# Optimization experiments

Hardware: AMD Instinct MI355X
Metric: run time of the kernel (lower is better)

## Reference

```python
import jax, jax.numpy as jnp
import numpy as np

GAMMA = 1.0
INPUT_DIM = 512
NUM_CENTERS = 4096
BATCH = 16384


def setup_inputs() -> dict:
    key = jax.random.key(0)
    kx, kc = jax.random.split(key)
    x = jax.random.normal(kx, (BATCH, INPUT_DIM), dtype=jnp.float32)
    centers = jax.random.normal(kc, (NUM_CENTERS, INPUT_DIM), dtype=jnp.float32)
    return {"x": x, "centers": centers}


def reference(x, centers):
    x_sq = jnp.sum(x * x, axis=-1, keepdims=True)            # [B, 1]
    c_sq = jnp.sum(centers * centers, axis=-1)               # [C]
    cross = jnp.einsum("bd,cd->bc", x, centers)              # [B, C]
    dist_sq = x_sq - 2.0 * cross + c_sq[None, :]
    return jnp.exp(-GAMMA * dist_sq)
```

## Files before the change

### kernel.cpp

```cpp
#include <hip/hip_runtime.h>
#include <stdint.h>

#define M_DIM 16384
#define N_DIM 4096
#define K_DIM 512

#define BM 128
#define BN 256
#define BK 128

typedef int v8i __attribute__((ext_vector_type(8)));
typedef float f32x16 __attribute__((ext_vector_type(16)));

typedef __attribute__((address_space(3))) uint32_t lds_u32_t;
typedef const __attribute__((address_space(1))) uint32_t glob_u32_t;

__device__ __forceinline__ void gload16(const void* g, void* l) {
    __builtin_amdgcn_global_load_lds((glob_u32_t*)g, (lds_u32_t*)l, 16, 0, 0);
}

__global__ __launch_bounds__(256)
void convert_norm_kernel(const float* __restrict__ X, const float* __restrict__ C,
                         uint8_t* __restrict__ Xf8, uint8_t* __restrict__ Cf8,
                         float* __restrict__ xsq, float* __restrict__ csq) {
    const int wave = threadIdx.x >> 6;
    const int lane = threadIdx.x & 63;
    const int row = blockIdx.x * 4 + wave;
    const float* src;
    uint8_t* dst;
    float* nrm;
    int r;
    if (row < M_DIM) { src = X; dst = Xf8; nrm = xsq; r = row; }
    else             { src = C; dst = Cf8; nrm = csq; r = row - M_DIM; }

    const float4* p = (const float4*)(src + (size_t)r * K_DIM) + lane * 2;
    float4 a = p[0], b = p[1];
    uint32_t lo = 0, hi = 0;
    lo = __builtin_amdgcn_cvt_pk_fp8_f32(a.x, a.y, lo, false);
    lo = __builtin_amdgcn_cvt_pk_fp8_f32(a.z, a.w, lo, true);
    hi = __builtin_amdgcn_cvt_pk_fp8_f32(b.x, b.y, hi, false);
    hi = __builtin_amdgcn_cvt_pk_fp8_f32(b.z, b.w, hi, true);
    *(uint2*)(dst + (size_t)r * K_DIM + lane * 8) = make_uint2(lo, hi);

    float s = a.x*a.x + a.y*a.y + a.z*a.z + a.w*a.w
            + b.x*b.x + b.y*b.y + b.z*b.z + b.w*b.w;
    #pragma unroll
    for (int off = 32; off > 0; off >>= 1) s += __shfl_down(s, off, 64);
    if (lane == 0) nrm[r] = s;
}

__global__ __launch_bounds__(256, 2)
void rbf_mfma_kernel(const uint8_t* __restrict__ A8, const uint8_t* __restrict__ B8,
                     const float* __restrict__ xsq, const float* __restrict__ csq,
                     float* __restrict__ out) {
    __shared__ uint8_t As[BM * BK];
    __shared__ uint8_t Bs[BN * BK];

    const int tid  = threadIdx.x;
    const int lane = tid & 63;
    const int wave = tid >> 6;
    const int h    = lane >> 5;
    const int r31  = lane & 31;

    const int bn = (blockIdx.x & 15) * BN;
    const int bm = (blockIdx.x >> 4) * BM;

    const int wm = (wave >> 1) * 64;
    const int wn = (wave & 1) * 128;

    const int sr  = tid >> 3;
    const int skc = ((tid & 7) - sr) & 7;
    const uint8_t* pA = A8 + (size_t)(bm + sr) * K_DIM + skc * 16;
    const uint8_t* pB = B8 + (size_t)(bn + sr) * K_DIM + skc * 16;
    uint8_t* AsW = As + wave * 1024;
    uint8_t* BsW = Bs + wave * 1024;

    f32x16 acc[2][4] = {};

    for (int k0 = 0; k0 < K_DIM; k0 += BK) {
        #pragma unroll
        for (int R = 0; R < 4; ++R)
            gload16(pA + k0 + (size_t)R * 32 * K_DIM, AsW + R * 4096);
        #pragma unroll
        for (int R = 0; R < 8; ++R)
            gload16(pB + k0 + (size_t)R * 32 * K_DIM, BsW + R * 4096);
        __syncthreads();

        #pragma unroll
        for (int ks = 0; ks < 2; ++ks) {
            v8i av[2], bv[4];
            #pragma unroll
            for (int i = 0; i < 2; ++i) {
                const int panel = (wm >> 5) + i;
                uint4 lo = *(const uint4*)(As + (panel * 256 + r31 * 8 + ((ks * 4 + 2 * h + 0 + r31) & 7)) * 16);
                uint4 hi = *(const uint4*)(As + (panel * 256 + r31 * 8 + ((ks * 4 + 2 * h + 1 + r31) & 7)) * 16);
                av[i] = (v8i){(int)lo.x, (int)lo.y, (int)lo.z, (int)lo.w,
                              (int)hi.x, (int)hi.y, (int)hi.z, (int)hi.w};
            }
            #pragma unroll
            for (int j = 0; j < 4; ++j) {
                const int panel = (wn >> 5) + j;
                uint4 lo = *(const uint4*)(Bs + (panel * 256 + r31 * 8 + ((ks * 4 + 2 * h + 0 + r31) & 7)) * 16);
                uint4 hi = *(const uint4*)(Bs + (panel * 256 + r31 * 8 + ((ks * 4 + 2 * h + 1 + r31) & 7)) * 16);
                bv[j] = (v8i){(int)lo.x, (int)lo.y, (int)lo.z, (int)lo.w,
                              (int)hi.x, (int)hi.y, (int)hi.z, (int)hi.w};
            }
            #pragma unroll
            for (int i = 0; i < 2; ++i)
                #pragma unroll
                for (int j = 0; j < 4; ++j)
                    acc[i][j] = __builtin_amdgcn_mfma_scale_f32_32x32x64_f8f6f4(
                        av[i], bv[j], acc[i][j],
                        0 , 0 ,
                        0, 0x7F7F7F7Fu ,
                        0, 0x7F7F7F7Fu );
        }
        __syncthreads();
    }

    float cs[4];
    #pragma unroll
    for (int j = 0; j < 4; ++j) cs[j] = csq[bn + wn + 32 * j + r31];

    #pragma unroll
    for (int i = 0; i < 2; ++i) {
        #pragma unroll
        for (int r = 0; r < 16; ++r) {
            const int gm = bm + wm + 32 * i + 4 * h + (r & 3) + 8 * (r >> 2);
            const float xs = xsq[gm];
            float* orow = out + (size_t)gm * N_DIM + bn + wn;
            #pragma unroll
            for (int j = 0; j < 4; ++j) {
                float d = xs - 2.0f * acc[i][j][r] + cs[j];
                orow[32 * j + r31] = __expf(-d);
            }
        }
    }
}

extern "C" void kernel_launch(void* const* d_in, const int* in_sizes, int n_in,
                              void* d_out, int out_size, void* d_ws, size_t ws_size,
                              hipStream_t stream) {
    const float* X = (const float*)d_in[0];
    const float* C = (const float*)d_in[1];
    float* out = (float*)d_out;

    uint8_t* Xf8 = (uint8_t*)d_ws;
    uint8_t* Cf8 = Xf8 + (size_t)M_DIM * K_DIM;
    float* xsq = (float*)(Cf8 + (size_t)N_DIM * K_DIM);
    float* csq = xsq + M_DIM;

    convert_norm_kernel<<<(M_DIM + N_DIM) / 4, 256, 0, stream>>>(X, C, Xf8, Cf8, xsq, csq);
    rbf_mfma_kernel<<<(M_DIM / BM) * (N_DIM / BN), 256, 0, stream>>>(Xf8, Cf8, xsq, csq, out);
}
```

Baseline: 308.9 us.

## Double-buffer LDS K-tiles and permute B rows for float4 output stores

Halves the K tile to 64 and double-buffers the A and B LDS tiles, so the next tile's global-to-LDS loads are issued before the current tile's MFMAs. This is meant to hide load latency and drops one barrier per iteration. B rows are loaded in a permuted order so each lane owns four consecutive output columns, letting the epilogue read csq with one float4 and write the output with 128-bit stores. The risk is more loop iterations with less work each, and LDS swizzle or row-mapping mistakes.

```diff
diff --git a/kernel.cpp b/kernel.cpp
--- a/kernel.cpp
+++ b/kernel.cpp
@@ -7,7 +7,7 @@
 
 #define BM 128
 #define BN 256
-#define BK 128
+#define BK 64
 
 typedef int v8i __attribute__((ext_vector_type(8)));
 typedef float f32x16 __attribute__((ext_vector_type(16)));
@@ -53,8 +53,8 @@
 void rbf_mfma_kernel(const uint8_t* __restrict__ A8, const uint8_t* __restrict__ B8,
                      const float* __restrict__ xsq, const float* __restrict__ csq,
                      float* __restrict__ out) {
-    __shared__ uint8_t As[BM * BK];
-    __shared__ uint8_t Bs[BN * BK];
+    __shared__ uint8_t As[2 * BM * BK];
+    __shared__ uint8_t Bs[2 * BN * BK];
 
     const int tid  = threadIdx.x;
     const int lane = tid & 63;
@@ -68,59 +68,78 @@
     const int wm = (wave >> 1) * 64;
     const int wn = (wave & 1) * 128;
 
-    const int sr  = tid >> 3;
-    const int skc = ((tid & 7) - sr) & 7;
-    const uint8_t* pA = A8 + (size_t)(bm + sr) * K_DIM + skc * 16;
-    const uint8_t* pB = B8 + (size_t)(bn + sr) * K_DIM + skc * 16;
-    uint8_t* AsW = As + wave * 1024;
-    uint8_t* BsW = Bs + wave * 1024;
+    const int tr = tid >> 2;
+    const int tc = tid & 3;
+    const int cc = (tc - tr) & 3;
+    const int b7 = tid >> 7;
+
+    const uint8_t* gA0 = A8 + (size_t)(bm + tr) * K_DIM + cc * 16;
+    const uint8_t* gA1 = gA0 + (size_t)64 * K_DIM;
+    const int brow = 4 * (tr & 31);
+    const uint8_t* gB[4];
+    #pragma unroll
+    for (int R = 0; R < 4; ++R) {
+        const int p = 2 * R + b7;
+        const int grow = bn + (p >> 2) * 128 + brow + (p & 3);
+        gB[R] = B8 + (size_t)grow * K_DIM + cc * 16;
+    }
+
+    {
+        uint8_t* aD = As + wave * 1024;
+        uint8_t* bD = Bs + wave * 1024;
+        gload16(gA0, aD);
+        gload16(gA1, aD + 4096);
+        #pragma unroll
+        for (int R = 0; R < 4; ++R) gload16(gB[R], bD + R * 4096);
+    }
+    int koff = 64;
+
+    const int s0 = ((2 * h + 0 + r31) & 3) * 16;
+    const int s1 = ((2 * h + 1 + r31) & 3) * 16;
+    const int aOff = (wave >> 1) * 2 * 2048 + r31 * 64;
+    const int bOff = (wave & 1) * 4 * 2048 + r31 * 64;
 
     f32x16 acc[2][4] = {};
 
-    for (int k0 = 0; k0 < K_DIM; k0 += BK) {
+    for (int kk = 0; kk < K_DIM / BK; ++kk) {
+        __syncthreads();
+        if (kk < K_DIM / BK - 1) {
+            uint8_t* aD = As + ((kk + 1) & 1) * 8192 + wave * 1024;
+            uint8_t* bD = Bs + ((kk + 1) & 1) * 16384 + wave * 1024;
+            gload16(gA0 + koff, aD);
+            gload16(gA1 + koff, aD + 4096);
+            #pragma unroll
+            for (int R = 0; R < 4; ++R) gload16(gB[R] + koff, bD + R * 4096);
+            koff += 64;
+        }
+        const uint8_t* aB = As + (kk & 1) * 8192 + aOff;
+        const uint8_t* bB = Bs + (kk & 1) * 16384 + bOff;
+        v8i av[2], bv[4];
         #pragma unroll
-        for (int R = 0; R < 4; ++R)
-            gload16(pA + k0 + (size_t)R * 32 * K_DIM, AsW + R * 4096);
+        for (int i = 0; i < 2; ++i) {
+            uint4 lo = *(const uint4*)(aB + i * 2048 + s0);
+            uint4 hi = *(const uint4*)(aB + i * 2048 + s1);
+            av[i] = (v8i){(int)lo.x, (int)lo.y, (int)lo.z, (int)lo.w,
+                          (int)hi.x, (int)hi.y, (int)hi.z, (int)hi.w};
+        }
         #pragma unroll
-        for (int R = 0; R < 8; ++R)
-            gload16(pB + k0 + (size_t)R * 32 * K_DIM, BsW + R * 4096);
-        __syncthreads();
-
+        for (int j = 0; j < 4; ++j) {
+            uint4 lo = *(const uint4*)(bB + j * 2048 + s0);
+            uint4 hi = *(const uint4*)(bB + j * 2048 + s1);
+            bv[j] = (v8i){(int)lo.x, (int)lo.y, (int)lo.z, (int)lo.w,
+                          (int)hi.x, (int)hi.y, (int)hi.z, (int)hi.w};
+        }
         #pragma unroll
-        for (int ks = 0; ks < 2; ++ks) {
-            v8i av[2], bv[4];
+        for (int i = 0; i < 2; ++i)
             #pragma unroll
-            for (int i = 0; i < 2; ++i) {
-                const int panel = (wm >> 5) + i;
-                uint4 lo = *(const uint4*)(As + (panel * 256 + r31 * 8 + ((ks * 4 + 2 * h + 0 + r31) & 7)) * 16);
-                uint4 hi = *(const uint4*)(As + (panel * 256 + r31 * 8 + ((ks * 4 + 2 * h + 1 + r31) & 7)) * 16);
-                av[i] = (v8i){(int)lo.x, (int)lo.y, (int)lo.z, (int)lo.w,
-                              (int)hi.x, (int)hi.y, (int)hi.z, (int)hi.w};
-            }
-            #pragma unroll
-            for (int j = 0; j < 4; ++j) {
-                const int panel = (wn >> 5) + j;
-                uint4 lo = *(const uint4*)(Bs + (panel * 256 + r31 * 8 + ((ks * 4 + 2 * h + 0 + r31) & 7)) * 16);
-                uint4 hi = *(const uint4*)(Bs + (panel * 256 + r31 * 8 + ((ks * 4 + 2 * h + 1 + r31) & 7)) * 16);
-                bv[j] = (v8i){(int)lo.x, (int)lo.y, (int)lo.z, (int)lo.w,
-                              (int)hi.x, (int)hi.y, (int)hi.z, (int)hi.w};
-            }
-            #pragma unroll
-            for (int i = 0; i < 2; ++i)
-                #pragma unroll
-                for (int j = 0; j < 4; ++j)
-                    acc[i][j] = __builtin_amdgcn_mfma_scale_f32_32x32x64_f8f6f4(
-                        av[i], bv[j], acc[i][j],
-                        0 , 0 ,
-                        0, 0x7F7F7F7Fu ,
-                        0, 0x7F7F7F7Fu );
-        }
-        __syncthreads();
+            for (int j = 0; j < 4; ++j)
+                acc[i][j] = __builtin_amdgcn_mfma_scale_f32_32x32x64_f8f6f4(
+                    av[i], bv[j], acc[i][j],
+                    0 , 0 ,
+                    0, 0x7F7F7F7Fu, 0, 0x7F7F7F7Fu);
     }
 
-    float cs[4];
-    #pragma unroll
-    for (int j = 0; j < 4; ++j) cs[j] = csq[bn + wn + 32 * j + r31];
+    const float4 cs4 = *(const float4*)(csq + bn + wn + 4 * r31);
 
     #pragma unroll
     for (int i = 0; i < 2; ++i) {
@@ -128,12 +147,12 @@
         for (int r = 0; r < 16; ++r) {
             const int gm = bm + wm + 32 * i + 4 * h + (r & 3) + 8 * (r >> 2);
             const float xs = xsq[gm];
-            float* orow = out + (size_t)gm * N_DIM + bn + wn;
-            #pragma unroll
-            for (int j = 0; j < 4; ++j) {
-                float d = xs - 2.0f * acc[i][j][r] + cs[j];
-                orow[32 * j + r31] = __expf(-d);
-            }
+            float4 o;
+            o.x = __expf(-(xs - 2.0f * acc[i][0][r] + cs4.x));
+            o.y = __expf(-(xs - 2.0f * acc[i][1][r] + cs4.y));
+            o.z = __expf(-(xs - 2.0f * acc[i][2][r] + cs4.z));
+            o.w = __expf(-(xs - 2.0f * acc[i][3][r] + cs4.w));
+            *(float4*)(out + (size_t)gm * N_DIM + bn + wn + 4 * r31) = o;
         }
     }
 }
```

New measurement: 316.6 us. +2.5%, slower.

## Prepack FP8 operands in MFMA fragment order and load directly from global

Applied to the files above, without the earlier changes.

The conversion kernel now writes X and centers in a panel layout that matches the MFMA operand fragments, so the GEMM kernel drops shared memory and barriers and reads each fragment straight from global memory. Center rows are permuted so each lane owns four consecutive output columns, letting the epilogue issue float4 stores and a single float4 load of the center norms. The change removes LDS staging and synchronisation, but every wave now fetches its operands from L2/global with no sharing between waves in the block, and there is no explicit prefetch to hide that latency.

```diff
diff --git a/kernel.cpp b/kernel.cpp
--- a/kernel.cpp
+++ b/kernel.cpp
@@ -7,31 +7,30 @@
 
 #define BM 128
 #define BN 256
-#define BK 128
 
 typedef int v8i __attribute__((ext_vector_type(8)));
 typedef float f32x16 __attribute__((ext_vector_type(16)));
 
-typedef __attribute__((address_space(3))) uint32_t lds_u32_t;
-typedef const __attribute__((address_space(1))) uint32_t glob_u32_t;
-
-__device__ __forceinline__ void gload16(const void* g, void* l) {
-    __builtin_amdgcn_global_load_lds((glob_u32_t*)g, (lds_u32_t*)l, 16, 0, 0);
-}
 
 __global__ __launch_bounds__(256)
 void convert_norm_kernel(const float* __restrict__ X, const float* __restrict__ C,
-                         uint8_t* __restrict__ Xf8, uint8_t* __restrict__ Cf8,
+                         uint8_t* __restrict__ Apack, uint8_t* __restrict__ Bpack,
                          float* __restrict__ xsq, float* __restrict__ csq) {
     const int wave = threadIdx.x >> 6;
     const int lane = threadIdx.x & 63;
     const int row = blockIdx.x * 4 + wave;
+
     const float* src;
     uint8_t* dst;
     float* nrm;
-    int r;
-    if (row < M_DIM) { src = X; dst = Xf8; nrm = xsq; r = row; }
-    else             { src = C; dst = Cf8; nrm = csq; r = row - M_DIM; }
+    int r, panel, slot;
+    if (row < M_DIM) {
+        src = X; dst = Apack; nrm = xsq; r = row;
+        panel = r >> 5; slot = r & 31;
+    } else {
+        src = C; dst = Bpack; nrm = csq; r = row - M_DIM;
+        panel = (r >> 7) * 4 + (r & 3); slot = (r >> 2) & 31;
+    }
 
     const float4* p = (const float4*)(src + (size_t)r * K_DIM) + lane * 2;
     float4 a = p[0], b = p[1];
@@ -40,22 +39,22 @@
     lo = __builtin_amdgcn_cvt_pk_fp8_f32(a.z, a.w, lo, true);
     hi = __builtin_amdgcn_cvt_pk_fp8_f32(b.x, b.y, hi, false);
     hi = __builtin_amdgcn_cvt_pk_fp8_f32(b.z, b.w, hi, true);
-    *(uint2*)(dst + (size_t)r * K_DIM + lane * 8) = make_uint2(lo, hi);
+
+    const size_t off = (size_t)(panel * 8 + (lane >> 3)) * 2048
+                     + ((lane >> 2) & 1) * 1024 + slot * 32 + (lane & 3) * 8;
+    *(uint2*)(dst + off) = make_uint2(lo, hi);
 
     float s = a.x*a.x + a.y*a.y + a.z*a.z + a.w*a.w
             + b.x*b.x + b.y*b.y + b.z*b.z + b.w*b.w;
     #pragma unroll
-    for (int off = 32; off > 0; off >>= 1) s += __shfl_down(s, off, 64);
+    for (int off2 = 32; off2 > 0; off2 >>= 1) s += __shfl_down(s, off2, 64);
     if (lane == 0) nrm[r] = s;
 }
 
 __global__ __launch_bounds__(256, 2)
-void rbf_mfma_kernel(const uint8_t* __restrict__ A8, const uint8_t* __restrict__ B8,
+void rbf_mfma_kernel(const uint8_t* __restrict__ Apack, const uint8_t* __restrict__ Bpack,
                      const float* __restrict__ xsq, const float* __restrict__ csq,
                      float* __restrict__ out) {
-    __shared__ uint8_t As[BM * BK];
-    __shared__ uint8_t Bs[BN * BK];
-
     const int tid  = threadIdx.x;
     const int lane = tid & 63;
     const int wave = tid >> 6;
@@ -68,59 +67,44 @@
     const int wm = (wave >> 1) * 64;
     const int wn = (wave & 1) * 128;
 
-    const int sr  = tid >> 3;
-    const int skc = ((tid & 7) - sr) & 7;
-    const uint8_t* pA = A8 + (size_t)(bm + sr) * K_DIM + skc * 16;
-    const uint8_t* pB = B8 + (size_t)(bn + sr) * K_DIM + skc * 16;
-    uint8_t* AsW = As + wave * 1024;
-    uint8_t* BsW = Bs + wave * 1024;
+    const int P0 = (bm + wm) >> 5;
+    const int Q0 = ((bn + wn) >> 7) * 4;
+
+    const uint8_t* aBase = Apack + (size_t)P0 * 8 * 2048 + h * 1024 + r31 * 32;
+    const uint8_t* bBase = Bpack + (size_t)Q0 * 8 * 2048 + h * 1024 + r31 * 32;
 
     f32x16 acc[2][4] = {};
 
-    for (int k0 = 0; k0 < K_DIM; k0 += BK) {
+    #pragma unroll
+    for (int ks = 0; ks < 8; ++ks) {
+        v8i av[2], bv[4];
         #pragma unroll
-        for (int R = 0; R < 4; ++R)
-            gload16(pA + k0 + (size_t)R * 32 * K_DIM, AsW + R * 4096);
+        for (int i = 0; i < 2; ++i) {
+            const uint8_t* p = aBase + (size_t)(i * 8 + ks) * 2048;
+            uint4 lo = *(const uint4*)(p);
+            uint4 hi = *(const uint4*)(p + 16);
+            av[i] = (v8i){(int)lo.x, (int)lo.y, (int)lo.z, (int)lo.w,
+                          (int)hi.x, (int)hi.y, (int)hi.z, (int)hi.w};
+        }
         #pragma unroll
-        for (int R = 0; R < 8; ++R)
-            gload16(pB + k0 + (size_t)R * 32 * K_DIM, BsW + R * 4096);
-        __syncthreads();
-
+        for (int j = 0; j < 4; ++j) {
+            const uint8_t* p = bBase + (size_t)(j * 8 + ks) * 2048;
+            uint4 lo = *(const uint4*)(p);
+            uint4 hi = *(const uint4*)(p + 16);
+            bv[j] = (v8i){(int)lo.x, (int)lo.y, (int)lo.z, (int)lo.w,
+                          (int)hi.x, (int)hi.y, (int)hi.z, (int)hi.w};
+        }
         #pragma unroll
-        for (int ks = 0; ks < 2; ++ks) {
-            v8i av[2], bv[4];
+        for (int i = 0; i < 2; ++i)
             #pragma unroll
-            for (int i = 0; i < 2; ++i) {
-                const int panel = (wm >> 5) + i;
-                uint4 lo = *(const uint4*)(As + (panel * 256 + r31 * 8 + ((ks * 4 + 2 * h + 0 + r31) & 7)) * 16);
-                uint4 hi = *(const uint4*)(As + (panel * 256 + r31 * 8 + ((ks * 4 + 2 * h + 1 + r31) & 7)) * 16);
-                av[i] = (v8i){(int)lo.x, (int)lo.y, (int)lo.z, (int)lo.w,
-                              (int)hi.x, (int)hi.y, (int)hi.z, (int)hi.w};
-            }
-            #pragma unroll
-            for (int j = 0; j < 4; ++j) {
-                const int panel = (wn >> 5) + j;
-                uint4 lo = *(const uint4*)(Bs + (panel * 256 + r31 * 8 + ((ks * 4 + 2 * h + 0 + r31) & 7)) * 16);
-                uint4 hi = *(const uint4*)(Bs + (panel * 256 + r31 * 8 + ((ks * 4 + 2 * h + 1 + r31) & 7)) * 16);
-                bv[j] = (v8i){(int)lo.x, (int)lo.y, (int)lo.z, (int)lo.w,
-                              (int)hi.x, (int)hi.y, (int)hi.z, (int)hi.w};
-            }
-            #pragma unroll
-            for (int i = 0; i < 2; ++i)
-                #pragma unroll
-                for (int j = 0; j < 4; ++j)
-                    acc[i][j] = __builtin_amdgcn_mfma_scale_f32_32x32x64_f8f6f4(
-                        av[i], bv[j], acc[i][j],
-                        0 , 0 ,
-                        0, 0x7F7F7F7Fu ,
-                        0, 0x7F7F7F7Fu );
-        }
-        __syncthreads();
+            for (int j = 0; j < 4; ++j)
+                acc[i][j] = __builtin_amdgcn_mfma_scale_f32_32x32x64_f8f6f4(
+                    av[i], bv[j], acc[i][j],
+                    0 , 0 ,
+                    0, 0x7F7F7F7Fu, 0, 0x7F7F7F7Fu);
     }
 
-    float cs[4];
-    #pragma unroll
-    for (int j = 0; j < 4; ++j) cs[j] = csq[bn + wn + 32 * j + r31];
+    const float4 cs4 = *(const float4*)(csq + bn + wn + 4 * r31);
 
     #pragma unroll
     for (int i = 0; i < 2; ++i) {
@@ -128,12 +112,12 @@
         for (int r = 0; r < 16; ++r) {
             const int gm = bm + wm + 32 * i + 4 * h + (r & 3) + 8 * (r >> 2);
             const float xs = xsq[gm];
-            float* orow = out + (size_t)gm * N_DIM + bn + wn;
-            #pragma unroll
-            for (int j = 0; j < 4; ++j) {
-                float d = xs - 2.0f * acc[i][j][r] + cs[j];
-                orow[32 * j + r31] = __expf(-d);
-            }
+            float4 o;
+            o.x = __expf(-(xs - 2.0f * acc[i][0][r] + cs4.x));
+            o.y = __expf(-(xs - 2.0f * acc[i][1][r] + cs4.y));
+            o.z = __expf(-(xs - 2.0f * acc[i][2][r] + cs4.z));
+            o.w = __expf(-(xs - 2.0f * acc[i][3][r] + cs4.w));
+            *(float4*)(out + (size_t)gm * N_DIM + bn + wn + 4 * r31) = o;
         }
     }
 }
@@ -145,11 +129,11 @@
     const float* C = (const float*)d_in[1];
     float* out = (float*)d_out;
 
-    uint8_t* Xf8 = (uint8_t*)d_ws;
-    uint8_t* Cf8 = Xf8 + (size_t)M_DIM * K_DIM;
-    float* xsq = (float*)(Cf8 + (size_t)N_DIM * K_DIM);
+    uint8_t* Apack = (uint8_t*)d_ws;
+    uint8_t* Bpack = Apack + (size_t)M_DIM * K_DIM;
+    float* xsq = (float*)(Bpack + (size_t)N_DIM * K_DIM);
     float* csq = xsq + M_DIM;
 
-    convert_norm_kernel<<<(M_DIM + N_DIM) / 4, 256, 0, stream>>>(X, C, Xf8, Cf8, xsq, csq);
-    rbf_mfma_kernel<<<(M_DIM / BM) * (N_DIM / BN), 256, 0, stream>>>(Xf8, Cf8, xsq, csq, out);
+    convert_norm_kernel<<<(M_DIM + N_DIM) / 4, 256, 0, stream>>>(X, C, Apack, Bpack, xsq, csq);
+    rbf_mfma_kernel<<<(M_DIM / BM) * (N_DIM / BN), 256, 0, stream>>>(Apack, Bpack, xsq, csq, out);
 }
```

After: 316.5 us. 2.5% more time.

## Permute B tile columns so lanes emit contiguous float4 nontemporal output stores

Applied to the files above, without the earlier changes.

Halves the N tile to 128 and gives each wave a 32x128 output slab. B rows are loaded into LDS in a permuted order so each lane's four accumulators map to four adjacent output columns. The epilogue can then write 16-byte vectorized nontemporal stores instead of scalar 4-byte stores, and the occupancy hint rises to 3 blocks per CU. The goal is cheaper writes of the large fp32 output. The cost is less operand reuse per block: B is now read once per 128 columns and A twice as often.

```diff
diff --git a/kernel.cpp b/kernel.cpp
--- a/kernel.cpp
+++ b/kernel.cpp
@@ -6,11 +6,12 @@
 #define K_DIM 512
 
 #define BM 128
-#define BN 256
+#define BN 128
 #define BK 128
 
 typedef int v8i __attribute__((ext_vector_type(8)));
 typedef float f32x16 __attribute__((ext_vector_type(16)));
+typedef float f32x4v __attribute__((ext_vector_type(4)));
 
 typedef __attribute__((address_space(3))) uint32_t lds_u32_t;
 typedef const __attribute__((address_space(1))) uint32_t glob_u32_t;
@@ -49,7 +50,7 @@
     if (lane == 0) nrm[r] = s;
 }
 
-__global__ __launch_bounds__(256, 2)
+__global__ __launch_bounds__(256, 3)
 void rbf_mfma_kernel(const uint8_t* __restrict__ A8, const uint8_t* __restrict__ B8,
                      const float* __restrict__ xsq, const float* __restrict__ csq,
                      float* __restrict__ out) {
@@ -62,79 +63,73 @@
     const int h    = lane >> 5;
     const int r31  = lane & 31;
 
-    const int bn = (blockIdx.x & 15) * BN;
-    const int bm = (blockIdx.x >> 4) * BM;
+    const int bn = (blockIdx.x & 31) * BN;
+    const int bm = (blockIdx.x >> 5) * BM;
 
-    const int wm = (wave >> 1) * 64;
-    const int wn = (wave & 1) * 128;
+    const int tr = tid >> 3;
+    const int tc = tid & 7;
+    const int cc = (tc - tr) & 7;
 
-    const int sr  = tid >> 3;
-    const int skc = ((tid & 7) - sr) & 7;
-    const uint8_t* pA = A8 + (size_t)(bm + sr) * K_DIM + skc * 16;
-    const uint8_t* pB = B8 + (size_t)(bn + sr) * K_DIM + skc * 16;
+    const uint8_t* gA = A8 + (size_t)(bm + tr) * K_DIM + cc * 16;
+    const uint8_t* gB = B8 + (size_t)(bn + 4 * tr) * K_DIM + cc * 16;
     uint8_t* AsW = As + wave * 1024;
     uint8_t* BsW = Bs + wave * 1024;
 
-    f32x16 acc[2][4] = {};
+    const uint8_t* aRow = As + (32 * wave + r31) * BK;
+    const uint8_t* bRow = Bs + r31 * BK;
 
-    for (int k0 = 0; k0 < K_DIM; k0 += BK) {
+    f32x16 acc[4] = {};
+
+    for (int kk = 0; kk < 4; ++kk) {
+        const int koff = kk * 128;
         #pragma unroll
-        for (int R = 0; R < 4; ++R)
-            gload16(pA + k0 + (size_t)R * 32 * K_DIM, AsW + R * 4096);
-        #pragma unroll
-        for (int R = 0; R < 8; ++R)
-            gload16(pB + k0 + (size_t)R * 32 * K_DIM, BsW + R * 4096);
+        for (int R = 0; R < 4; ++R) {
+            gload16(gA + koff + (size_t)R * 32 * K_DIM, AsW + R * 4096);
+            gload16(gB + koff + (size_t)R * K_DIM, BsW + R * 4096);
+        }
         __syncthreads();
 
         #pragma unroll
-        for (int ks = 0; ks < 2; ++ks) {
-            v8i av[2], bv[4];
-            #pragma unroll
-            for (int i = 0; i < 2; ++i) {
-                const int panel = (wm >> 5) + i;
-                uint4 lo = *(const uint4*)(As + (panel * 256 + r31 * 8 + ((ks * 4 + 2 * h + 0 + r31) & 7)) * 16);
-                uint4 hi = *(const uint4*)(As + (panel * 256 + r31 * 8 + ((ks * 4 + 2 * h + 1 + r31) & 7)) * 16);
-                av[i] = (v8i){(int)lo.x, (int)lo.y, (int)lo.z, (int)lo.w,
-                              (int)hi.x, (int)hi.y, (int)hi.z, (int)hi.w};
+        for (int ksl = 0; ksl < 2; ++ksl) {
+            const int c0 = ksl * 4 + 2 * h;
+            const int s0 = ((c0 + 0 + r31) & 7) * 16;
+            const int s1 = ((c0 + 1 + r31) & 7) * 16;
+            v8i av, bv[4];
+            {
+                uint4 lo = *(const uint4*)(aRow + s0);
+                uint4 hi = *(const uint4*)(aRow + s1);
+                av = (v8i){(int)lo.x, (int)lo.y, (int)lo.z, (int)lo.w,
+                           (int)hi.x, (int)hi.y, (int)hi.z, (int)hi.w};
             }
             #pragma unroll
             for (int j = 0; j < 4; ++j) {
-                const int panel = (wn >> 5) + j;
-                uint4 lo = *(const uint4*)(Bs + (panel * 256 + r31 * 8 + ((ks * 4 + 2 * h + 0 + r31) & 7)) * 16);
-                uint4 hi = *(const uint4*)(Bs + (panel * 256 + r31 * 8 + ((ks * 4 + 2 * h + 1 + r31) & 7)) * 16);
+                uint4 lo = *(const uint4*)(bRow + j * 32 * BK + s0);
+                uint4 hi = *(const uint4*)(bRow + j * 32 * BK + s1);
                 bv[j] = (v8i){(int)lo.x, (int)lo.y, (int)lo.z, (int)lo.w,
                               (int)hi.x, (int)hi.y, (int)hi.z, (int)hi.w};
             }
             #pragma unroll
-            for (int i = 0; i < 2; ++i)
-                #pragma unroll
-                for (int j = 0; j < 4; ++j)
-                    acc[i][j] = __builtin_amdgcn_mfma_scale_f32_32x32x64_f8f6f4(
-                        av[i], bv[j], acc[i][j],
-                        0 , 0 ,
-                        0, 0x7F7F7F7Fu ,
-                        0, 0x7F7F7F7Fu );
+            for (int j = 0; j < 4; ++j)
+                acc[j] = __builtin_amdgcn_mfma_scale_f32_32x32x64_f8f6f4(
+                    av, bv[j], acc[j],
+                    0 , 0 ,
+                    0, 0x7F7F7F7Fu, 0, 0x7F7F7F7Fu);
         }
         __syncthreads();
     }
 
-    float cs[4];
-    #pragma unroll
-    for (int j = 0; j < 4; ++j) cs[j] = csq[bn + wn + 32 * j + r31];
+    const float4 cs4 = *(const float4*)(csq + bn + 4 * r31);
 
     #pragma unroll
-    for (int i = 0; i < 2; ++i) {
-        #pragma unroll
-        for (int r = 0; r < 16; ++r) {
-            const int gm = bm + wm + 32 * i + 4 * h + (r & 3) + 8 * (r >> 2);
-            const float xs = xsq[gm];
-            float* orow = out + (size_t)gm * N_DIM + bn + wn;
-            #pragma unroll
-            for (int j = 0; j < 4; ++j) {
-                float d = xs - 2.0f * acc[i][j][r] + cs[j];
-                orow[32 * j + r31] = __expf(-d);
-            }
-        }
+    for (int r = 0; r < 16; ++r) {
+        const int gm = bm + 32 * wave + 4 * h + (r & 3) + 8 * (r >> 2);
+        const float xs = xsq[gm];
+        f32x4v o;
+        o.x = __expf(-(xs - 2.0f * acc[0][r] + cs4.x));
+        o.y = __expf(-(xs - 2.0f * acc[1][r] + cs4.y));
+        o.z = __expf(-(xs - 2.0f * acc[2][r] + cs4.z));
+        o.w = __expf(-(xs - 2.0f * acc[3][r] + cs4.w));
+        __builtin_nontemporal_store(o, (f32x4v*)(out + (size_t)gm * N_DIM + bn + 4 * r31));
     }
 }
 
```

Result: faster. 300.1 us (-2.9%).
